# Optimization experiments

Measured on AMD Instinct MI355X. Metric: run time of the kernel, lower is better.

## Reference

```python
import jax, jax.numpy as jnp
import numpy as np

N_QUBITS = 10
CNOT_CHAIN = [(i, i + 1) for i in range(N_QUBITS - 1)] + [(N_QUBITS - 1, 0)]


def setup_inputs() -> dict:
    key = jax.random.key(0)
    k1, k2, k3, k4 = jax.random.split(key, 4)
    B, S, E, F = 32, 512, 1024, 4096
    return {
        "x": jax.random.normal(k1, (B, S, N_QUBITS), dtype=jnp.float32),
        "q_params": jax.random.normal(k2, (N_QUBITS,), dtype=jnp.float32),
        "W1": jax.random.normal(k3, (F, N_QUBITS), dtype=jnp.float32) / np.sqrt(N_QUBITS),
        "W2": jax.random.normal(k4, (E, F), dtype=jnp.float32) / np.sqrt(F),
    }


def _simulate(angles):
    """Batched state-vector sim: RX(angle_i) on wire i from |0..0>, CNOT ring,
    then Pauli-Z expectation on every wire. angles: [N, n] -> [N, n]."""
    N, n = angles.shape
    half = 0.5 * angles
    c, s = jnp.cos(half), jnp.sin(half)
    # RX(theta)|0> = [cos(theta/2), -i sin(theta/2)]; per-qubit states [N, n, 2]
    qs = jnp.stack([c.astype(jnp.complex64), (-1j) * s.astype(jnp.complex64)], axis=-1)
    # product state via iterated Kronecker product -> [N, 2^n]
    state = qs[:, 0]
    for i in range(1, n):
        state = (state[:, :, None] * qs[:, i][:, None, :]).reshape(N, -1)
    state = state.reshape((N,) + (2,) * n)  # axis i+1 <-> wire i
    # CNOT(src, tgt): flip target amplitudes on the control=1 half (permutation)
    for src, tgt in CNOT_CHAIN:
        s0, s1 = jnp.split(state, 2, axis=src + 1)
        state = jnp.concatenate([s0, jnp.flip(s1, axis=tgt + 1)], axis=src + 1)
    probs = (state.real ** 2 + state.imag ** 2).reshape(N, -1)  # [N, 2^n]
    # <Z_i> = sum_k p_k * (1 - 2*bit_i(k)); wire 0 is the most-significant bit
    bits = (jnp.arange(2 ** n)[:, None] >> (n - 1 - jnp.arange(n))) & 1
    signs = (1 - 2 * bits).astype(probs.dtype)  # [2^n, n]
    return probs @ signs


def reference(x, q_params, W1, W2):
    B, S, n = x.shape
    # back-to-back RX on the same wire commute: angles add
    angles = (x + q_params).reshape(B * S, n)
    q_out = _simulate(angles).reshape(B, S, n)
    # dropout is identity at inference; it sits before ReLU and is a no-op here
    h = jax.nn.relu(q_out @ W1.T)  # [B, S, ffn_dim]
    return h @ W2.T  # [B, S, embed_dim]
```

## Files before the change

### kernel.cpp

```cpp
#include <hip/hip_runtime.h>
#include <hip/hip_bf16.h>

typedef __bf16 bf16x8 __attribute__((ext_vector_type(8)));
typedef float f32x16 __attribute__((ext_vector_type(16)));

#define NQ     10
#define M_ROWS 16384
#define N_COLS 1024
#define K_DIM  4096

__device__ __forceinline__ void gload_lds16(const __hip_bfloat16* g, __hip_bfloat16* l) {
  __builtin_amdgcn_global_load_lds(
      (const __attribute__((address_space(1))) void*)g,
      (__attribute__((address_space(3))) void*)l,
      16, 0, 0);
}

__global__ void __launch_bounds__(256) prep(const float* __restrict__ W1,
                                            const float* __restrict__ W2,
                                            const float* __restrict__ x,
                                            const float* __restrict__ qp,
                                            __hip_bfloat16* __restrict__ W2b,
                                            __hip_bfloat16* __restrict__ Wq,
                                            __hip_bfloat16* __restrict__ Qb) {
  const int b = blockIdx.x;
  const int tid = threadIdx.x;
  if (b < 4096) {
    int i = (b * 256 + tid) * 4;
    float4 v = *(const float4*)(W2 + i);
    union { __hip_bfloat16 h[4]; uint2 u; } p;
    p.h[0] = __float2bfloat16(v.x);
    p.h[1] = __float2bfloat16(v.y);
    p.h[2] = __float2bfloat16(v.z);
    p.h[3] = __float2bfloat16(v.w);
    *(uint2*)(W2b + i) = p.u;
  } else if (b < 4112) {
    int kcol = (b - 4096) * 256 + tid;
    union { __hip_bfloat16 h[16]; uint4 u[2]; } p;
#pragma unroll
    for (int j = 0; j < NQ; j++) p.h[j] = __float2bfloat16(W1[kcol * NQ + j]);
#pragma unroll
    for (int j = NQ; j < 16; j++) p.h[j] = __float2bfloat16(0.f);
    *(uint4*)(Wq + kcol * 16) = p.u[0];
    *(uint4*)(Wq + kcol * 16 + 8) = p.u[1];
  } else {
    int row = (b - 4112) * 256 + tid;
    float c[NQ];
#pragma unroll
    for (int j = 0; j < NQ; j++) c[j] = cosf(x[row * NQ + j] + qp[j]);
    float q[NQ];
    float prod19 = 1.f;
#pragma unroll
    for (int j = 1; j < NQ; j++) prod19 *= c[j];
    q[0] = prod19;
    float pref = c[0];
#pragma unroll
    for (int k = 1; k < NQ; k++) { pref *= c[k]; q[k] = pref; }
    union { __hip_bfloat16 h[16]; uint4 u[2]; } p;
#pragma unroll
    for (int j = 0; j < NQ; j++) p.h[j] = __float2bfloat16(q[j]);
#pragma unroll
    for (int j = NQ; j < 16; j++) p.h[j] = __float2bfloat16(0.f);
    *(uint4*)(Qb + row * 16) = p.u[0];
    *(uint4*)(Qb + row * 16 + 8) = p.u[1];
  }
}

__global__ void __launch_bounds__(256, 2) gemm_fused(const __hip_bfloat16* __restrict__ Qb,
                                                     const __hip_bfloat16* __restrict__ Wq,
                                                     const __hip_bfloat16* __restrict__ B,
                                                     float* __restrict__ C) {
  __shared__ __align__(16) __hip_bfloat16 As[256 * 64];
  __shared__ __align__(16) __hip_bfloat16 Bs[128 * 64];

  const int tid  = threadIdx.x;
  const int wave = tid >> 6;
  const int lane = tid & 63;
  const int l31  = lane & 31;
  const int l5   = lane >> 5;
  const int l7   = l31 & 7;
  const int wm   = (wave & 1) * 128;
  const int wn   = (wave >> 1) * 64;

  const int L    = blockIdx.x;
  const int xcd  = L & 7;
  const int idx  = L >> 3;
  const int col0 = (idx >> 3) * 128;
  const int row0 = ((xcd << 3) | (idx & 7)) * 256;

  const int ldrow = lane >> 3;
  const int ldc   = (((lane & 7) ^ ldrow) << 3);

  bf16x8 qb[2];
#pragma unroll
  for (int i = 0; i < 2; i++)
    qb[i] = *(const bf16x8*)(Qb + (row0 + (2 * wave + i) * 32 + l31) * 16 + l5 * 8);

  f32x16 acc[4][2];
#pragma unroll
  for (int i = 0; i < 4; i++)
#pragma unroll
    for (int j = 0; j < 2; j++)
#pragma unroll
      for (int r = 0; r < 16; r++) acc[i][j][r] = 0.f;

  for (int k0 = 0; k0 < K_DIM; k0 += 64) {
#pragma unroll
    for (int i = 0; i < 4; i++)
      gload_lds16(B + (col0 + wave * 32 + i * 8 + ldrow) * K_DIM + k0 + ldc,
                  Bs + (wave * 4 + i) * 512);

    bf16x8 wq[2];
#pragma unroll
    for (int kt = 0; kt < 2; kt++)
      wq[kt] = *(const bf16x8*)(Wq + (k0 + kt * 32 + l31) * 16 + l5 * 8);

#pragma unroll
    for (int kt = 0; kt < 2; kt++) {
#pragma unroll
      for (int i = 0; i < 2; i++) {
        f32x16 d;
#pragma unroll
        for (int r = 0; r < 16; r++) d[r] = 0.f;
        d = __builtin_amdgcn_mfma_f32_32x32x16_bf16(wq[kt], qb[i], d, 0, 0, 0);
        const int hrow = (2 * wave + i) * 32 + l31;
#pragma unroll
        for (int q = 0; q < 4; q++) {
          union { __hip_bfloat16 h[4]; ushort4 u; } p;
#pragma unroll
          for (int r = 0; r < 4; r++)
            p.h[r] = __float2bfloat16(fmaxf(d[4 * q + r], 0.f));
          const int slot = (kt * 4 + q) ^ (l31 & 7);
          *(ushort4*)(As + hrow * 64 + slot * 8 + 4 * l5) = p.u;
        }
      }
    }
    __syncthreads();

#pragma unroll
    for (int kki = 0; kki < 4; kki++) {
      const int ch = (((2 * kki + l5) ^ l7) << 3);
      bf16x8 af[4], bb[2];
#pragma unroll
      for (int f = 0; f < 4; f++)
        af[f] = *(const bf16x8*)(As + (wm + f * 32 + l31) * 64 + ch);
#pragma unroll
      for (int f = 0; f < 2; f++)
        bb[f] = *(const bf16x8*)(Bs + (wn + f * 32 + l31) * 64 + ch);
#pragma unroll
      for (int fm = 0; fm < 4; fm++)
#pragma unroll
        for (int fn = 0; fn < 2; fn++)
          acc[fm][fn] = __builtin_amdgcn_mfma_f32_32x32x16_bf16(af[fm], bb[fn], acc[fm][fn], 0, 0, 0);
    }
    __syncthreads();
  }

#pragma unroll
  for (int fm = 0; fm < 4; fm++) {
#pragma unroll
    for (int fn = 0; fn < 2; fn++) {
      const int colb = col0 + wn + fn * 32 + l31;
      const int rowb = row0 + wm + fm * 32 + 4 * l5;
#pragma unroll
      for (int reg = 0; reg < 16; reg++) {
        int row = rowb + (reg & 3) + 8 * (reg >> 2);
        C[row * N_COLS + colb] = acc[fm][fn][reg];
      }
    }
  }
}

extern "C" void kernel_launch(void* const* d_in, const int* in_sizes, int n_in,
                              void* d_out, int out_size, void* d_ws, size_t ws_size,
                              hipStream_t stream) {
  const float* x  = (const float*)d_in[0];
  const float* qp = (const float*)d_in[1];
  const float* W1 = (const float*)d_in[2];
  const float* W2 = (const float*)d_in[3];
  float* out = (float*)d_out;

  char* ws = (char*)d_ws;
  __hip_bfloat16* W2b = (__hip_bfloat16*)ws;
  __hip_bfloat16* Wq  = (__hip_bfloat16*)(ws + 8388608);
  __hip_bfloat16* Qb  = (__hip_bfloat16*)(ws + 8519680);

  prep<<<4176, 256, 0, stream>>>(W1, W2, x, qp, W2b, Wq, Qb);
  gemm_fused<<<(M_ROWS / 256) * (N_COLS / 128), 256, 0, stream>>>(Qb, Wq, W2b, out);
}
```

Before: 228.5 us.

## Double-buffer LDS and pipeline fused hidden-tile GEMM with 256x256 tiles

The fused GEMM moves to 512-thread blocks computing 256x256 output tiles, with a grid of 256 blocks mapped to XCDs. The A (ReLU hidden) and B (W2) LDS tiles are double-buffered. The next tile's global-to-LDS loads and the small MFMA hidden-layer computation are interleaved with the four MFMA phases of the current tile, using raw s_barrier, s_setprio and explicit vmcnt waits. The goal is to hide load latency and cut the full __syncthreads stalls of the previous single-buffered loop. In exchange it uses 128KB of LDS, which allows only one block per CU. It also prefetches past the end of K into adjacent workspace memory, and that data is never used.

```diff
diff --git a/kernel.cpp b/kernel.cpp
--- a/kernel.cpp
+++ b/kernel.cpp
@@ -15,6 +15,8 @@
       (__attribute__((address_space(3))) void*)l,
       16, 0, 0);
 }
+
+#define MEMF asm volatile("" ::: "memory")
 
 __global__ void __launch_bounds__(256) prep(const float* __restrict__ W1,
                                             const float* __restrict__ W2,
@@ -66,12 +68,12 @@
   }
 }
 
-__global__ void __launch_bounds__(256, 2) gemm_fused(const __hip_bfloat16* __restrict__ Qb,
+__global__ void __launch_bounds__(512, 2) gemm_fused(const __hip_bfloat16* __restrict__ Qb,
                                                      const __hip_bfloat16* __restrict__ Wq,
                                                      const __hip_bfloat16* __restrict__ B,
                                                      float* __restrict__ C) {
-  __shared__ __align__(16) __hip_bfloat16 As[256 * 64];
-  __shared__ __align__(16) __hip_bfloat16 Bs[128 * 64];
+  __shared__ __align__(16) __hip_bfloat16 As[2][256 * 64];
+  __shared__ __align__(16) __hip_bfloat16 Bs[2][256 * 64];
 
   const int tid  = threadIdx.x;
   const int wave = tid >> 6;
@@ -79,22 +81,19 @@
   const int l31  = lane & 31;
   const int l5   = lane >> 5;
   const int l7   = l31 & 7;
-  const int wm   = (wave & 1) * 128;
-  const int wn   = (wave >> 1) * 64;
+  const int wm   = (wave >> 2) * 128;
+  const int wn   = (wave & 3) * 64;
 
   const int L    = blockIdx.x;
   const int xcd  = L & 7;
   const int idx  = L >> 3;
-  const int col0 = (idx >> 3) * 128;
-  const int row0 = ((xcd << 3) | (idx & 7)) * 256;
+  const int col0 = (xcd >> 1) * 256;
+  const int row0 = (((xcd & 1) << 5) + idx) * 256;
 
   const int ldrow = lane >> 3;
   const int ldc   = (((lane & 7) ^ ldrow) << 3);
 
-  bf16x8 qb[2];
-#pragma unroll
-  for (int i = 0; i < 2; i++)
-    qb[i] = *(const bf16x8*)(Qb + (row0 + (2 * wave + i) * 32 + l31) * 16 + l5 * 8);
+  const bf16x8 qb = *(const bf16x8*)(Qb + (row0 + wave * 32 + l31) * 16 + l5 * 8);
 
   f32x16 acc[4][2];
 #pragma unroll
@@ -104,56 +103,74 @@
 #pragma unroll
       for (int r = 0; r < 16; r++) acc[i][j][r] = 0.f;
 
-  for (int k0 = 0; k0 < K_DIM; k0 += 64) {
-#pragma unroll
-    for (int i = 0; i < 4; i++)
-      gload_lds16(B + (col0 + wave * 32 + i * 8 + ldrow) * K_DIM + k0 + ldc,
-                  Bs + (wave * 4 + i) * 512);
-
-    bf16x8 wq[2];
-#pragma unroll
-    for (int kt = 0; kt < 2; kt++)
-      wq[kt] = *(const bf16x8*)(Wq + (k0 + kt * 32 + l31) * 16 + l5 * 8);
-
-#pragma unroll
-    for (int kt = 0; kt < 2; kt++) {
-#pragma unroll
-      for (int i = 0; i < 2; i++) {
-        f32x16 d;
-#pragma unroll
-        for (int r = 0; r < 16; r++) d[r] = 0.f;
-        d = __builtin_amdgcn_mfma_f32_32x32x16_bf16(wq[kt], qb[i], d, 0, 0, 0);
-        const int hrow = (2 * wave + i) * 32 + l31;
-#pragma unroll
-        for (int q = 0; q < 4; q++) {
-          union { __hip_bfloat16 h[4]; ushort4 u; } p;
-#pragma unroll
-          for (int r = 0; r < 4; r++)
-            p.h[r] = __float2bfloat16(fmaxf(d[4 * q + r], 0.f));
-          const int slot = (kt * 4 + q) ^ (l31 & 7);
-          *(ushort4*)(As + hrow * 64 + slot * 8 + 4 * l5) = p.u;
-        }
-      }
-    }
-    __syncthreads();
-
-#pragma unroll
-    for (int kki = 0; kki < 4; kki++) {
-      const int ch = (((2 * kki + l5) ^ l7) << 3);
-      bf16x8 af[4], bb[2];
-#pragma unroll
-      for (int f = 0; f < 4; f++)
-        af[f] = *(const bf16x8*)(As + (wm + f * 32 + l31) * 64 + ch);
-#pragma unroll
-      for (int f = 0; f < 2; f++)
-        bb[f] = *(const bf16x8*)(Bs + (wn + f * 32 + l31) * 64 + ch);
-#pragma unroll
-      for (int fm = 0; fm < 4; fm++)
-#pragma unroll
-        for (int fn = 0; fn < 2; fn++)
-          acc[fm][fn] = __builtin_amdgcn_mfma_f32_32x32x16_bf16(af[fm], bb[fn], acc[fm][fn], 0, 0, 0);
-    }
-    __syncthreads();
+#define WQF(t, kt) (*(const bf16x8*)(Wq + ((t) * 64 + (kt) * 32 + l31) * 16 + l5 * 8))
+
+#define STAGE(bw, ts, i)                                                              \
+  gload_lds16(B + (col0 + wave * 32 + (i) * 8 + ldrow) * K_DIM + (ts) * 64 + ldc,     \
+              &Bs[bw][(wave * 32 + (i) * 8) * 64])
+
+#define MINI(bw, wqf, kt) do {                                                        \
+    f32x16 d_;                                                                        \
+    _Pragma("unroll") for (int r_ = 0; r_ < 16; r_++) d_[r_] = 0.f;                   \
+    d_ = __builtin_amdgcn_mfma_f32_32x32x16_bf16((wqf), qb, d_, 0, 0, 0);             \
+    const int hb_ = (wave * 32 + l31) * 64;                                           \
+    _Pragma("unroll") for (int q_ = 0; q_ < 4; q_++) {                                \
+      union { __hip_bfloat16 h[4]; ushort4 u; } p_;                                   \
+      _Pragma("unroll") for (int r_ = 0; r_ < 4; r_++)                                \
+        p_.h[r_] = __float2bfloat16(fmaxf(d_[4 * q_ + r_], 0.f));                     \
+      *(ushort4*)(&As[bw][hb_ + ((((kt) * 4 + q_) ^ l7) << 3) + 4 * l5]) = p_.u;      \
+    }                                                                                 \
+  } while (0)
+
+#define MFMA_BF16 __builtin_amdgcn_mfma_f32_32x32x16_bf16
+#define NOTAIL
+#define TAILW asm volatile("s_waitcnt vmcnt(2)" ::: "memory")
+
+#define PHASE(br, kki, TAIL) do {                                                     \
+    const int ch_ = (((2 * (kki) + l5) ^ l7) << 3);                                   \
+    const bf16x8 af0 = *(const bf16x8*)(&As[br][(wm +  0 + l31) * 64 + ch_]);         \
+    const bf16x8 af1 = *(const bf16x8*)(&As[br][(wm + 32 + l31) * 64 + ch_]);         \
+    const bf16x8 af2 = *(const bf16x8*)(&As[br][(wm + 64 + l31) * 64 + ch_]);         \
+    const bf16x8 af3 = *(const bf16x8*)(&As[br][(wm + 96 + l31) * 64 + ch_]);         \
+    const bf16x8 bb0 = *(const bf16x8*)(&Bs[br][(wn +  0 + l31) * 64 + ch_]);         \
+    const bf16x8 bb1 = *(const bf16x8*)(&Bs[br][(wn + 32 + l31) * 64 + ch_]);         \
+    MEMF; __builtin_amdgcn_s_barrier(); MEMF;                                         \
+    __builtin_amdgcn_s_setprio(1);                                                    \
+    acc[0][0] = MFMA_BF16(af0, bb0, acc[0][0], 0, 0, 0);                              \
+    acc[1][0] = MFMA_BF16(af1, bb0, acc[1][0], 0, 0, 0);                              \
+    acc[2][0] = MFMA_BF16(af2, bb0, acc[2][0], 0, 0, 0);                              \
+    acc[3][0] = MFMA_BF16(af3, bb0, acc[3][0], 0, 0, 0);                              \
+    acc[0][1] = MFMA_BF16(af0, bb1, acc[0][1], 0, 0, 0);                              \
+    acc[1][1] = MFMA_BF16(af1, bb1, acc[1][1], 0, 0, 0);                              \
+    acc[2][1] = MFMA_BF16(af2, bb1, acc[2][1], 0, 0, 0);                              \
+    acc[3][1] = MFMA_BF16(af3, bb1, acc[3][1], 0, 0, 0);                              \
+    __builtin_amdgcn_s_setprio(0);                                                    \
+    TAIL;                                                                             \
+    MEMF; __builtin_amdgcn_s_barrier(); MEMF;                                         \
+  } while (0)
+
+#define TILE(br, bw, wqu0, wqu1, wqp0, wqp1, t) do {                                  \
+    STAGE(bw, (t) + 1, 0); STAGE(bw, (t) + 1, 1);                                     \
+    MINI(bw, wqu0, 0);                                                                \
+    PHASE(br, 0, NOTAIL);                                                             \
+    STAGE(bw, (t) + 1, 2); STAGE(bw, (t) + 1, 3);                                     \
+    MINI(bw, wqu1, 1);                                                                \
+    PHASE(br, 1, NOTAIL);                                                             \
+    PHASE(br, 2, NOTAIL);                                                             \
+    wqp0 = WQF((t) + 2, 0); wqp1 = WQF((t) + 2, 1);                                   \
+    PHASE(br, 3, TAILW);                                                              \
+  } while (0)
+
+  STAGE(0, 0, 0); STAGE(0, 0, 1); STAGE(0, 0, 2); STAGE(0, 0, 3);
+  bf16x8 wqA0 = WQF(0, 0), wqA1 = WQF(0, 1);
+  bf16x8 wqB0 = WQF(1, 0), wqB1 = WQF(1, 1);
+  MINI(0, wqA0, 0);
+  MINI(0, wqA1, 1);
+  __syncthreads();
+
+  for (int u = 0; u < 32; u++) {
+    TILE(0, 1, wqB0, wqB1, wqA0, wqA1, 2 * u);
+    TILE(1, 0, wqA0, wqA1, wqB0, wqB1, 2 * u + 1);
   }
 
 #pragma unroll
@@ -186,5 +203,5 @@
   __hip_bfloat16* Qb  = (__hip_bfloat16*)(ws + 8519680);
 
   prep<<<4176, 256, 0, stream>>>(W1, W2, x, qp, W2b, Wq, Qb);
-  gemm_fused<<<(M_ROWS / 256) * (N_COLS / 128), 256, 0, stream>>>(Qb, Wq, W2b, out);
-}
+  gemm_fused<<<256, 512, 0, stream>>>(Qb, Wq, W2b, out);
+}
```

After: 248.8 us. +8.9%, slower.

## Build ReLU hidden fragments in registers via permlane swap; double-buffer B tile

Applied to the files above, without the earlier changes.

The first-layer MFMA output is now turned straight into A-operand fragments for the main GEMM. The ReLU'd results are packed to bf16 pairs and rearranged across lanes with v_permlane32_swap, so the As shared-memory tile and its write/read round trip are gone. The B tile is double-buffered in LDS, and the next tile's loads are issued before the current tile's compute, leaving one barrier per K-step instead of two. The cost is redundant first-layer MFMAs across the waves that share the same rows, plus more registers. The final iteration also prefetches one tile past the end of K, reading into adjacent workspace.

```diff
diff --git a/kernel.cpp b/kernel.cpp
--- a/kernel.cpp
+++ b/kernel.cpp
@@ -15,6 +15,20 @@
       (__attribute__((address_space(3))) void*)l,
       16, 0, 0);
 }
+
+__device__ __forceinline__ unsigned pkrelu(float a, float b) {
+  union { __hip_bfloat162 h; unsigned u; } r;
+  r.h = __float22bfloat162_rn(float2{fmaxf(a, 0.f), fmaxf(b, 0.f)});
+  return r.u;
+}
+
+__device__ __forceinline__ bf16x8 mkfrag(unsigned a, unsigned b, unsigned c, unsigned d) {
+  union { unsigned u[4]; bf16x8 v; } f;
+  f.u[0] = a; f.u[1] = b; f.u[2] = c; f.u[3] = d;
+  return f.v;
+}
+
+#define PLSWAP(a, b) asm("v_permlane32_swap_b32 %0, %1" : "+v"(a), "+v"(b))
 
 __global__ void __launch_bounds__(256) prep(const float* __restrict__ W1,
                                             const float* __restrict__ W2,
@@ -70,8 +84,7 @@
                                                      const __hip_bfloat16* __restrict__ Wq,
                                                      const __hip_bfloat16* __restrict__ B,
                                                      float* __restrict__ C) {
-  __shared__ __align__(16) __hip_bfloat16 As[256 * 64];
-  __shared__ __align__(16) __hip_bfloat16 Bs[128 * 64];
+  __shared__ __align__(16) __hip_bfloat16 Bs[2][128 * 64];
 
   const int tid  = threadIdx.x;
   const int wave = tid >> 6;
@@ -91,10 +104,10 @@
   const int ldrow = lane >> 3;
   const int ldc   = (((lane & 7) ^ ldrow) << 3);
 
-  bf16x8 qb[2];
-#pragma unroll
-  for (int i = 0; i < 2; i++)
-    qb[i] = *(const bf16x8*)(Qb + (row0 + (2 * wave + i) * 32 + l31) * 16 + l5 * 8);
+  const bf16x8 qb0 = *(const bf16x8*)(Qb + (row0 + wm +  0 + l31) * 16 + l5 * 8);
+  const bf16x8 qb1 = *(const bf16x8*)(Qb + (row0 + wm + 32 + l31) * 16 + l5 * 8);
+  const bf16x8 qb2 = *(const bf16x8*)(Qb + (row0 + wm + 64 + l31) * 16 + l5 * 8);
+  const bf16x8 qb3 = *(const bf16x8*)(Qb + (row0 + wm + 96 + l31) * 16 + l5 * 8);
 
   f32x16 acc[4][2];
 #pragma unroll
@@ -104,56 +117,65 @@
 #pragma unroll
       for (int r = 0; r < 16; r++) acc[i][j][r] = 0.f;
 
-  for (int k0 = 0; k0 < K_DIM; k0 += 64) {
-#pragma unroll
-    for (int i = 0; i < 4; i++)
-      gload_lds16(B + (col0 + wave * 32 + i * 8 + ldrow) * K_DIM + k0 + ldc,
-                  Bs + (wave * 4 + i) * 512);
-
-    bf16x8 wq[2];
-#pragma unroll
-    for (int kt = 0; kt < 2; kt++)
-      wq[kt] = *(const bf16x8*)(Wq + (k0 + kt * 32 + l31) * 16 + l5 * 8);
-
-#pragma unroll
-    for (int kt = 0; kt < 2; kt++) {
-#pragma unroll
-      for (int i = 0; i < 2; i++) {
-        f32x16 d;
-#pragma unroll
-        for (int r = 0; r < 16; r++) d[r] = 0.f;
-        d = __builtin_amdgcn_mfma_f32_32x32x16_bf16(wq[kt], qb[i], d, 0, 0, 0);
-        const int hrow = (2 * wave + i) * 32 + l31;
-#pragma unroll
-        for (int q = 0; q < 4; q++) {
-          union { __hip_bfloat16 h[4]; ushort4 u; } p;
-#pragma unroll
-          for (int r = 0; r < 4; r++)
-            p.h[r] = __float2bfloat16(fmaxf(d[4 * q + r], 0.f));
-          const int slot = (kt * 4 + q) ^ (l31 & 7);
-          *(ushort4*)(As + hrow * 64 + slot * 8 + 4 * l5) = p.u;
-        }
-      }
-    }
-    __syncthreads();
-
-#pragma unroll
-    for (int kki = 0; kki < 4; kki++) {
-      const int ch = (((2 * kki + l5) ^ l7) << 3);
-      bf16x8 af[4], bb[2];
-#pragma unroll
-      for (int f = 0; f < 4; f++)
-        af[f] = *(const bf16x8*)(As + (wm + f * 32 + l31) * 64 + ch);
-#pragma unroll
-      for (int f = 0; f < 2; f++)
-        bb[f] = *(const bf16x8*)(Bs + (wn + f * 32 + l31) * 64 + ch);
-#pragma unroll
-      for (int fm = 0; fm < 4; fm++)
-#pragma unroll
-        for (int fn = 0; fn < 2; fn++)
-          acc[fm][fn] = __builtin_amdgcn_mfma_f32_32x32x16_bf16(af[fm], bb[fn], acc[fm][fn], 0, 0, 0);
-    }
-    __syncthreads();
+  bf16x8 fr0[2], fr1[2], fr2[2], fr3[2];
+
+#define MFMA_BF16 __builtin_amdgcn_mfma_f32_32x32x16_bf16
+
+#define WQF(t, kt) (*(const bf16x8*)(Wq + ((t) * 64 + (kt) * 32 + l31) * 16 + l5 * 8))
+
+#define STAGE(bw, ts, i)                                                              \
+  gload_lds16(B + (col0 + wave * 32 + (i) * 8 + ldrow) * K_DIM + (ts) * 64 + ldc,     \
+              &Bs[bw][(wave * 32 + (i) * 8) * 64])
+
+#define MINIFR(QB, WQ, FR) do {                                                       \
+    f32x16 d_;                                                                        \
+    _Pragma("unroll") for (int r_ = 0; r_ < 16; r_++) d_[r_] = 0.f;                   \
+    d_ = MFMA_BF16(WQ, QB, d_, 0, 0, 0);                                              \
+    unsigned w0 = pkrelu(d_[0],  d_[1]),  w1 = pkrelu(d_[2],  d_[3]);                 \
+    unsigned w2 = pkrelu(d_[4],  d_[5]),  w3 = pkrelu(d_[6],  d_[7]);                 \
+    unsigned w4 = pkrelu(d_[8],  d_[9]),  w5 = pkrelu(d_[10], d_[11]);                \
+    unsigned w6 = pkrelu(d_[12], d_[13]), w7 = pkrelu(d_[14], d_[15]);                \
+    PLSWAP(w0, w2); PLSWAP(w1, w3);                                                   \
+    PLSWAP(w4, w6); PLSWAP(w5, w7);                                                   \
+    FR[0] = mkfrag(w0, w1, w2, w3);                                                   \
+    FR[1] = mkfrag(w4, w5, w6, w7);                                                   \
+  } while (0)
+
+#define MAINK(cur, kki, fi) do {                                                      \
+    const int ch_ = (((2 * (kki) + l5) ^ l7) << 3);                                   \
+    const bf16x8 bb0 = *(const bf16x8*)(&Bs[cur][(wn +  0 + l31) * 64 + ch_]);        \
+    const bf16x8 bb1 = *(const bf16x8*)(&Bs[cur][(wn + 32 + l31) * 64 + ch_]);        \
+    acc[0][0] = MFMA_BF16(fr0[fi], bb0, acc[0][0], 0, 0, 0);                          \
+    acc[1][0] = MFMA_BF16(fr1[fi], bb0, acc[1][0], 0, 0, 0);                          \
+    acc[2][0] = MFMA_BF16(fr2[fi], bb0, acc[2][0], 0, 0, 0);                          \
+    acc[3][0] = MFMA_BF16(fr3[fi], bb0, acc[3][0], 0, 0, 0);                          \
+    acc[0][1] = MFMA_BF16(fr0[fi], bb1, acc[0][1], 0, 0, 0);                          \
+    acc[1][1] = MFMA_BF16(fr1[fi], bb1, acc[1][1], 0, 0, 0);                          \
+    acc[2][1] = MFMA_BF16(fr2[fi], bb1, acc[2][1], 0, 0, 0);                          \
+    acc[3][1] = MFMA_BF16(fr3[fi], bb1, acc[3][1], 0, 0, 0);                          \
+  } while (0)
+
+#define TILE(cur, nxt, WQ0, WQ1, WQP0, WQP1, t) do {                                  \
+    STAGE(nxt, (t) + 1, 0); STAGE(nxt, (t) + 1, 1);                                   \
+    STAGE(nxt, (t) + 1, 2); STAGE(nxt, (t) + 1, 3);                                   \
+    WQP0 = WQF((t) + 1, 0); WQP1 = WQF((t) + 1, 1);                                   \
+    MINIFR(qb0, WQ0, fr0); MINIFR(qb1, WQ0, fr1);                                     \
+    MINIFR(qb2, WQ0, fr2); MINIFR(qb3, WQ0, fr3);                                     \
+    MAINK(cur, 0, 0); MAINK(cur, 1, 1);                                               \
+    MINIFR(qb0, WQ1, fr0); MINIFR(qb1, WQ1, fr1);                                     \
+    MINIFR(qb2, WQ1, fr2); MINIFR(qb3, WQ1, fr3);                                     \
+    MAINK(cur, 2, 0); MAINK(cur, 3, 1);                                               \
+    __syncthreads();                                                                  \
+  } while (0)
+
+  STAGE(0, 0, 0); STAGE(0, 0, 1); STAGE(0, 0, 2); STAGE(0, 0, 3);
+  bf16x8 wqC0 = WQF(0, 0), wqC1 = WQF(0, 1);
+  bf16x8 wqN0, wqN1;
+  __syncthreads();
+
+  for (int u = 0; u < 32; u++) {
+    TILE(0, 1, wqC0, wqC1, wqN0, wqN1, 2 * u);
+    TILE(1, 0, wqN0, wqN1, wqC0, wqC1, 2 * u + 1);
   }
 
 #pragma unroll
```

Result: slower. 280.2 us (+22.6%).
